# Kernel optimization log

Measured on AMD Instinct MI355X. Metric: run time of the kernel, lower is better.

## Reference

```python
import jax, jax.numpy as jnp
import numpy as np

B, S, D = 4, 2048, 1024
MULT = 4
INNER = MULT * D
E = 4          # n_expert
K = 1          # top-k
ALPHA = 0.5


def setup_inputs() -> dict:
    key = jax.random.key(0)
    ks = jax.random.split(key, 8)
    std = 0.02
    x = jax.random.normal(ks[0], (B, S, D), jnp.float32)
    W1 = jax.random.normal(ks[1], (D, INNER), jnp.float32) * std
    b1 = jnp.zeros((INNER,), jnp.float32)
    W2 = jax.random.normal(ks[2], (INNER, D), jnp.float32) * std
    b2 = jnp.zeros((D,), jnp.float32)
    Wg = jax.random.normal(ks[3], (D, E), jnp.float32) * std
    ew1 = jax.random.normal(ks[4], (E, D, INNER), jnp.float32) * std
    ew3 = jax.random.normal(ks[5], (E, D, INNER), jnp.float32) * std
    ew2 = jax.random.normal(ks[6], (E, INNER, D), jnp.float32) * std
    return {"x": x, "W1": W1, "b1": b1, "W2": W2, "b2": b2,
            "Wg": Wg, "ew1": ew1, "ew3": ew3, "ew2": ew2}


def reference(x, W1, b1, W2, b2, Wg, ew1, ew3, ew2):
    # Dense branch: Linear -> GELU (exact, torch default) -> Linear
    y_dense = jax.nn.gelu(x @ W1 + b1, approximate=False) @ W2 + b2

    # MoE branch: top-k softmax routing, SwiGLU experts
    logits = x @ Wg                                   # [B,S,E]
    probs = jax.nn.softmax(logits, axis=-1)
    topv, topi = jax.lax.top_k(probs, K)              # [B,S,K]
    gates = topv / jnp.sum(topv, axis=-1, keepdims=True)  # renormalize top-k
    onehot = jax.nn.one_hot(topi, E, dtype=x.dtype)   # [B,S,K,E]
    combine = jnp.sum(gates[..., None] * onehot, axis=-2)  # [B,S,E]

    y_moe = jnp.zeros_like(x)
    for e in range(E):  # small fixed expert count
        h = jax.nn.silu(x @ ew1[e]) * (x @ ew3[e])    # [B,S,INNER]
        y_moe = y_moe + combine[..., e:e + 1] * (h @ ew2[e])

    # Load-balancing aux loss: E * sum_e f_e * P_e
    frac = jnp.mean(jnp.sum(onehot, axis=-2), axis=(0, 1)) / K  # [E]
    pmean = jnp.mean(probs, axis=(0, 1))                        # [E]
    aux = E * jnp.sum(frac * pmean)

    y = ALPHA * y_dense + (1.0 - ALPHA) * y_moe
    return (y, aux)
```

## Files before the change

### kernel.cpp

```cpp
#include <hip/hip_runtime.h>
#include <hip/hip_bf16.h>


static constexpr int MT = 8192;
static constexpr int DD = 1024;
static constexpr int DI = 4096;

typedef float f32x4 __attribute__((ext_vector_type(4)));
typedef __bf16 bf16x8 __attribute__((ext_vector_type(8)));
typedef unsigned short u16;

__device__ __forceinline__ u16 f2bf(float f) {
    union { __hip_bfloat16 b; u16 u; } v;
    v.b = __float2bfloat16(f);
    return v.u;
}
__device__ __forceinline__ float bf2f(u16 u) {
    union { float f; unsigned i; } v;
    v.i = ((unsigned)u) << 16;
    return v.f;
}

__device__ __forceinline__ void gload_lds16(const void* g, void* l) {
    __builtin_amdgcn_global_load_lds(
        (const __attribute__((address_space(1))) void*)g,
        (__attribute__((address_space(3))) void*)l, 16, 0, 0);
}

__device__ __forceinline__ float gelu_f(float v) {
    return 0.5f * v * (1.0f + erff(v * 0.70710678118654752f));
}
__device__ __forceinline__ float silu_f(float v) {
    return v / (1.0f + expf(-v));
}

#define FENCE() asm volatile("" ::: "memory")
#define BARRIER() do { FENCE(); __builtin_amdgcn_s_barrier(); FENCE(); } while (0)
#define WAIT_LGKM0() asm volatile("s_waitcnt lgkmcnt(0)" ::: "memory")

__device__ __forceinline__ void transpose_tile(
    const float* __restrict__ s, u16* __restrict__ d, int K, int N,
    int pack, int packOff) {
    __shared__ u16 t[64][72];
    int n0 = blockIdx.x * 64, k0 = blockIdx.y * 64;
    int tid = threadIdx.x;
    int c = tid & 15;
    int r = tid >> 4;
#pragma unroll
    for (int p = 0; p < 4; ++p) {
        int k = r + p * 16;
        float4 v = *(const float4*)(s + (size_t)(k0 + k) * N + n0 + c * 4);
        t[c * 4 + 0][k] = f2bf(v.x);
        t[c * 4 + 1][k] = f2bf(v.y);
        t[c * 4 + 2][k] = f2bf(v.z);
        t[c * 4 + 3][k] = f2bf(v.w);
    }
    __syncthreads();
    int n = tid >> 2, kc = (tid & 3) * 16;
    const uint4* p0 = (const uint4*)&t[n][kc];
    uint4 a = p0[0], b = p0[1];
    int gn = n0 + n;
    int dr = pack ? ((gn >> 5) * 64 + (gn & 31) + packOff) : gn;
    uint4* o = (uint4*)(d + (size_t)dr * K + k0 + kc);
    o[0] = a; o[1] = b;
}

__global__ void __launch_bounds__(256) transpose_up(
    const float* __restrict__ W1, const float* __restrict__ ew1,
    const float* __restrict__ ew3, u16* __restrict__ W1t,
    u16* __restrict__ ew13t) {
    int z = blockIdx.z;
    if (z == 0) {
        transpose_tile(W1, W1t, DD, DI, 0, 0);
    } else if (z <= 4) {
        transpose_tile(ew1 + (size_t)(z - 1) * DD * DI,
                       ew13t + (size_t)(z - 1) * 2 * DD * DI, DD, DI, 1, 0);
    } else {
        transpose_tile(ew3 + (size_t)(z - 5) * DD * DI,
                       ew13t + (size_t)(z - 5) * 2 * DD * DI, DD, DI, 1, 32);
    }
}

__global__ void __launch_bounds__(256) transpose_dn(
    const float* __restrict__ W2, const float* __restrict__ ew2,
    u16* __restrict__ W2t, u16* __restrict__ ew2t) {
    int z = blockIdx.z;
    if (z == 0) {
        transpose_tile(W2, W2t, DI, DD, 0, 0);
    } else {
        transpose_tile(ew2 + (size_t)(z - 1) * DI * DD,
                       ew2t + (size_t)(z - 1) * DI * DD, DI, DD, 0, 0);
    }
}

__global__ void __launch_bounds__(256) gate_kernel(
    const float* __restrict__ x, const float* __restrict__ Wg,
    float* __restrict__ psum_blk, int* __restrict__ expertA) {
    int w = threadIdx.x >> 6, l = threadIdx.x & 63;
    int t = blockIdx.x * 4 + w;
    const float* xr = x + (size_t)t * DD;
    double a0 = 0, a1 = 0, a2 = 0, a3 = 0;
#pragma unroll
    for (int i = 0; i < 4; ++i) {
        int k = i * 256 + l * 4;
        float4 xv = *(const float4*)(xr + k);
        float4 w0 = *(const float4*)(Wg + (size_t)(k + 0) * 4);
        float4 w1 = *(const float4*)(Wg + (size_t)(k + 1) * 4);
        float4 w2 = *(const float4*)(Wg + (size_t)(k + 2) * 4);
        float4 w3 = *(const float4*)(Wg + (size_t)(k + 3) * 4);
        a0 += (double)xv.x * w0.x + (double)xv.y * w1.x + (double)xv.z * w2.x + (double)xv.w * w3.x;
        a1 += (double)xv.x * w0.y + (double)xv.y * w1.y + (double)xv.z * w2.y + (double)xv.w * w3.y;
        a2 += (double)xv.x * w0.z + (double)xv.y * w1.z + (double)xv.z * w2.z + (double)xv.w * w3.z;
        a3 += (double)xv.x * w0.w + (double)xv.y * w1.w + (double)xv.z * w2.w + (double)xv.w * w3.w;
    }
#pragma unroll
    for (int o = 32; o; o >>= 1) {
        a0 += __shfl_down(a0, o); a1 += __shfl_down(a1, o);
        a2 += __shfl_down(a2, o); a3 += __shfl_down(a3, o);
    }
    __shared__ float wps[4][4];
    if (l == 0) {
        double lg[4] = {a0, a1, a2, a3};
        int best = 0;
#pragma unroll
        for (int e = 1; e < 4; ++e) if (lg[e] > lg[best]) best = e;
        double m = lg[best], s = 0, p[4];
#pragma unroll
        for (int e = 0; e < 4; ++e) { p[e] = exp(lg[e] - m); s += p[e]; }
#pragma unroll
        for (int e = 0; e < 4; ++e) wps[w][e] = (float)(p[e] / s);
        expertA[t] = best;
    }
    __syncthreads();
    if (threadIdx.x < 4)
        psum_blk[blockIdx.x * 4 + threadIdx.x] =
            wps[0][threadIdx.x] + wps[1][threadIdx.x] + wps[2][threadIdx.x] + wps[3][threadIdx.x];
}

__global__ void __launch_bounds__(1024) build_lists(
    const int* __restrict__ expertA, const float* __restrict__ psum_blk,
    int* __restrict__ dstArr, int* __restrict__ rev,
    int* __restrict__ offsets, float* __restrict__ auxOut) {
    __shared__ int sc[4][1024];
    __shared__ float fs[1024];
    __shared__ float psum_s[4];
    __shared__ int tot_s[4], off_s[4];
    int tid = threadIdx.x;
    int le[8]; int c[4] = {0, 0, 0, 0};
#pragma unroll
    for (int i = 0; i < 8; ++i) { int e = expertA[tid * 8 + i]; le[i] = e; c[e]++; }
#pragma unroll
    for (int e = 0; e < 4; ++e) sc[e][tid] = c[e];
    __syncthreads();
    for (int o = 1; o < 1024; o <<= 1) {
        int v[4];
#pragma unroll
        for (int e = 0; e < 4; ++e) v[e] = (tid >= o) ? sc[e][tid - o] : 0;
        __syncthreads();
#pragma unroll
        for (int e = 0; e < 4; ++e) if (tid >= o) sc[e][tid] += v[e];
        __syncthreads();
    }
    if (tid == 0) {
        int o = 0;
#pragma unroll
        for (int e = 0; e < 4; ++e) {
            tot_s[e] = sc[e][1023]; off_s[e] = o; offsets[e] = o; o += tot_s[e];
        }
        offsets[4] = o;
    }
    __syncthreads();
    int base[4];
#pragma unroll
    for (int e = 0; e < 4; ++e) base[e] = off_s[e] + sc[e][tid] - c[e];
#pragma unroll
    for (int i = 0; i < 8; ++i) {
        int e = le[i]; int d = base[e]++; int t = tid * 8 + i;
        dstArr[t] = d; rev[d] = t;
    }
    float ps[4];
#pragma unroll
    for (int e = 0; e < 4; ++e)
        ps[e] = psum_blk[(2 * tid) * 4 + e] + psum_blk[(2 * tid + 1) * 4 + e];
    for (int e = 0; e < 4; ++e) {
        fs[tid] = ps[e]; __syncthreads();
        for (int o = 512; o; o >>= 1) { if (tid < o) fs[tid] += fs[tid + o]; __syncthreads(); }
        if (tid == 0) psum_s[e] = fs[0];
        __syncthreads();
    }
    if (tid == 0) {
        float a = 0;
#pragma unroll
        for (int e = 0; e < 4; ++e)
            a += ((float)tot_s[e] * (1.f / 8192.f)) * (psum_s[e] * (1.f / 8192.f));
        auxOut[0] = 4.f * a;
    }
}

__global__ void __launch_bounds__(256) gather_kernel(
    const float* __restrict__ x, const int* __restrict__ dstArr,
    u16* __restrict__ xg) {
    int w = threadIdx.x >> 6, l = threadIdx.x & 63;
    int t = blockIdx.x * 4 + w;
    int dst = dstArr[t];
    const float* xr = x + (size_t)t * DD;
#pragma unroll
    for (int i = 0; i < 4; ++i) {
        int k = i * 256 + l * 4;
        float4 v = *(const float4*)(xr + k);
        ushort4 u;
        u.x = f2bf(v.x); u.y = f2bf(v.y); u.z = f2bf(v.z); u.w = f2bf(v.w);
        *(ushort4*)(xg + (size_t)dst * DD + k) = u;
    }
}

template <int MODE, int NF>
__global__ void __launch_bounds__(512, 2) gemm8(
    const u16* __restrict__ A, const u16* __restrict__ Bw,
    const float* __restrict__ bias,
    u16* __restrict__ outB, float* __restrict__ outF,
    const int* __restrict__ offsets, const int* __restrict__ rev,
    int N, int K) {
    constexpr int BN   = NF * 64;
    constexpr int WCW  = NF * 16;
    constexpr int AELT = 2 * 256 * 32;
    constexpr int BUFE = AELT + 2 * BN * 32;
    constexpr int NIB  = NF / 2;
    __shared__ u16 lds[2 * BUFE];

    const int tid = threadIdx.x;
    const int w = tid >> 6, l = tid & 63;
    const int lr = l & 15, lg = l >> 4;
    const int wr = w >> 2, wc = w & 3;

    int rowBase, rowsValid = 256;
    const u16* Bp = Bw;
    if constexpr (MODE >= 2) {
        int e = blockIdx.z;
        int off = offsets[e], cnt = offsets[e + 1] - off;
        if ((int)blockIdx.y * 256 >= cnt) return;
        rowBase = off + blockIdx.y * 256;
        rowsValid = cnt - (int)blockIdx.y * 256;
        if (rowsValid > 256) rowsValid = 256;
        Bp = Bw + (size_t)e * ((size_t)2 * DD * DI);
    } else {
        rowBase = blockIdx.y * 256;
    }
    const int colBase = blockIdx.x * BN;
    const int NT = K >> 6;

    auto stageA = [&](int kt, int b, int ks) {
        const int kk = (kt << 6) + (ks << 5);
#pragma unroll
        for (int i = 0; i < 2; ++i) {
            int o = ((w << 1) + i) * 512 + (l << 3);
            int o2 = o ^ (((o >> 8) & 1) << 4);
            gload_lds16(A + (size_t)(rowBase + (o2 >> 5)) * K + kk + (o2 & 31),
                        &lds[b * BUFE + ks * 8192 + ((w << 1) + i) * 512]);
        }
    };
    auto stageB = [&](int kt, int b, int ks) {
        const int kk = (kt << 6) + (ks << 5);
#pragma unroll
        for (int i = 0; i < NIB; ++i) {
            int o = (w * NIB + i) * 512 + (l << 3);
            int o2 = o ^ (((o >> 8) & 1) << 4);
            gload_lds16(Bp + (size_t)(colBase + (o2 >> 5)) * K + kk + (o2 & 31),
                        &lds[b * BUFE + AELT + ks * (BN * 32) + (w * NIB + i) * 512]);
        }
    };

#define WAIT_VMB() do { \
    if constexpr (NF == 4) asm volatile("s_waitcnt vmcnt(4)" ::: "memory"); \
    else                   asm volatile("s_waitcnt vmcnt(3)" ::: "memory"); \
} while (0)

#define READBF(b_, ks_) do { \
    _Pragma("unroll") \
    for (int n = 0; n < NF; ++n) { \
        int e_ = (wc * WCW + n * 16 + lr) * 32 + lg * 8; \
        e_ ^= ((e_ >> 8) & 1) << 4; \
        bf[n] = *(const bf16x8*)&lds[(b_) * BUFE + AELT + (ks_) * (BN * 32) + e_]; \
    } \
} while (0)

#define READAF(b_, ks_, mq_) do { \
    _Pragma("unroll") \
    for (int m = 0; m < 4; ++m) { \
        int e_ = (wr * 128 + ((mq_) * 4 + m) * 16 + lr) * 32 + lg * 8; \
        e_ ^= ((e_ >> 8) & 1) << 4; \
        af[m] = *(const bf16x8*)&lds[(b_) * BUFE + (ks_) * 8192 + e_]; \
    } \
} while (0)

#define DOMFMA(mq_) do { \
    __builtin_amdgcn_s_setprio(1); \
    _Pragma("unroll") \
    for (int m = 0; m < 4; ++m) \
    _Pragma("unroll") \
    for (int n = 0; n < NF; ++n) \
        acc[(mq_) * 4 + m][n] = __builtin_amdgcn_mfma_f32_16x16x32_bf16( \
            bf[n], af[m], acc[(mq_) * 4 + m][n], 0, 0, 0); \
    __builtin_amdgcn_s_setprio(0); \
} while (0)

    f32x4 acc[8][NF];
#pragma unroll
    for (int m = 0; m < 8; ++m)
#pragma unroll
        for (int n = 0; n < NF; ++n) acc[m][n] = (f32x4){0.f, 0.f, 0.f, 0.f};
    bf16x8 af[4], bf[NF];

    stageA(0, 0, 0); stageB(0, 0, 0); stageA(0, 0, 1); stageB(0, 0, 1);
    stageA(1, 1, 0); stageB(1, 1, 0);
    WAIT_VMB();
    BARRIER();

    for (int t = 0; t < NT; ++t) {
        const int cb = t & 1, nb = cb ^ 1;
        const int tp1 = (t + 1 < NT) ? t + 1 : NT - 1;
        const int tp2 = (t + 2 < NT) ? t + 2 : NT - 1;
        READBF(cb, 0); READAF(cb, 0, 0); stageA(tp1, nb, 1);
        BARRIER(); WAIT_LGKM0(); DOMFMA(0); BARRIER();
        READAF(cb, 0, 1); stageB(tp1, nb, 1);
        BARRIER(); WAIT_LGKM0(); DOMFMA(1); BARRIER();
        READBF(cb, 1); READAF(cb, 1, 0); stageA(tp2, cb, 0);
        BARRIER(); WAIT_LGKM0(); DOMFMA(0); BARRIER();
        READAF(cb, 1, 1); stageB(tp2, cb, 0);
        BARRIER(); WAIT_LGKM0(); DOMFMA(1);
        WAIT_VMB();
        BARRIER();
    }

#pragma unroll
    for (int m = 0; m < 8; ++m) {
        int rloc = wr * 128 + m * 16 + lr;
        if (MODE >= 2 && rloc >= rowsValid) continue;
        size_t grow = (size_t)(rowBase + rloc);
        if constexpr (MODE == 2) {
#pragma unroll
            for (int n = 0; n < 2; ++n) {
                int col = (colBase >> 1) + wc * 32 + n * 16 + lg * 4;
                f32x4 v1 = acc[m][n], v3 = acc[m][n + 2];
                ushort4 u;
                u.x = f2bf(silu_f(v1[0]) * v3[0]);
                u.y = f2bf(silu_f(v1[1]) * v3[1]);
                u.z = f2bf(silu_f(v1[2]) * v3[2]);
                u.w = f2bf(silu_f(v1[3]) * v3[3]);
                *(ushort4*)(outB + grow * N + col) = u;
            }
        } else {
#pragma unroll
            for (int n = 0; n < NF; ++n) {
                int col = colBase + wc * WCW + n * 16 + lg * 4;
                f32x4 v = acc[m][n];
                f32x4 bb = *(const f32x4*)(bias + col);
                ushort4 u;
                u.x = f2bf(gelu_f(v[0] + bb[0]));
                u.y = f2bf(gelu_f(v[1] + bb[1]));
                u.z = f2bf(gelu_f(v[2] + bb[2]));
                u.w = f2bf(gelu_f(v[3] + bb[3]));
                *(ushort4*)(outB + grow * N + col) = u;
            }
        }
    }
#undef WAIT_VMB
#undef READBF
#undef READAF
#undef DOMFMA
}

__global__ void __launch_bounds__(256) gemm97sp(
    const u16* __restrict__ Ad, const u16* __restrict__ Ag,
    const u16* __restrict__ W2t, const u16* __restrict__ ew2t,
    u16* __restrict__ yA, float* __restrict__ y,
    const int* __restrict__ offsets, const int* __restrict__ rev) {
    __shared__ u16 ldsA[128 * 32];
    __shared__ u16 ldsB[128 * 32];
    int tid = threadIdx.x, w = tid >> 6, l = tid & 63;
    int wr = w >> 1, wc = w & 1;

    int wg = blockIdx.x;
    int c = wg & 7;
    int s = wg >> 3;
    int x = s & 7;
    int p = c + ((s >> 3) << 3);

    const u16* Ap;
    const u16* Bp;
    int rowBase, rowsValid = 128;
    bool dense = (p < 64);
    if (dense) {
        rowBase = p * 128;
        Ap = Ad; Bp = W2t;
    } else {
        int pm = p - 64;
        int e = pm >> 6, yl = pm & 63;
        int off = offsets[e], cnt = offsets[e + 1] - off;
        if (yl * 128 >= cnt) return;
        rowBase = off + yl * 128;
        rowsValid = cnt - yl * 128;
        if (rowsValid > 128) rowsValid = 128;
        Ap = Ag; Bp = ew2t + (size_t)e * DD * DI;
    }
    int colBase = x * 128;

    f32x4 acc[4][4];
#pragma unroll
    for (int m = 0; m < 4; ++m)
#pragma unroll
        for (int n = 0; n < 4; ++n) acc[m][n] = (f32x4){0.f, 0.f, 0.f, 0.f};

    int lr = l & 15, lg = l >> 4;
    int ar = l >> 2, ac = (l & 3) * 8;

#pragma unroll 1
    for (int kt = 0; kt < DI / 32; ++kt) {
        int k0 = kt << 5;
        const u16* ga = Ap + (size_t)(rowBase + w * 32 + ar) * DI + k0 + ac;
        gload_lds16(ga, &ldsA[(w * 32) * 32]);
        gload_lds16(ga + (size_t)16 * DI, &ldsA[(w * 32 + 16) * 32]);
        const u16* gb = Bp + (size_t)(colBase + w * 32 + ar) * DI + k0 + ac;
        gload_lds16(gb, &ldsB[(w * 32) * 32]);
        gload_lds16(gb + (size_t)16 * DI, &ldsB[(w * 32 + 16) * 32]);
        __syncthreads();
        bf16x8 af[4], bfr[4];
#pragma unroll
        for (int m = 0; m < 4; ++m)
            af[m] = *(const bf16x8*)&ldsA[(wr * 64 + m * 16 + lr) * 32 + lg * 8];
#pragma unroll
        for (int n = 0; n < 4; ++n)
            bfr[n] = *(const bf16x8*)&ldsB[(wc * 64 + n * 16 + lr) * 32 + lg * 8];
#pragma unroll
        for (int m = 0; m < 4; ++m)
#pragma unroll
            for (int n = 0; n < 4; ++n)
                acc[m][n] = __builtin_amdgcn_mfma_f32_16x16x32_bf16(
                    bfr[n], af[m], acc[m][n], 0, 0, 0);
        __syncthreads();
    }

#pragma unroll
    for (int m = 0; m < 4; ++m) {
        int rloc = wr * 64 + m * 16 + lr;
        if (rloc >= rowsValid) continue;
        int r = rowBase + rloc;
#pragma unroll
        for (int n = 0; n < 4; ++n) {
            int col = colBase + wc * 64 + n * 16 + lg * 4;
            f32x4 v = acc[m][n];
            if (dense) {
                ushort4 u;
                u.x = f2bf(v[0]); u.y = f2bf(v[1]);
                u.z = f2bf(v[2]); u.w = f2bf(v[3]);
                *(ushort4*)(yA + (size_t)r * DD + col) = u;
            } else {
                int tok = rev[r];
                f32x4 rr;
#pragma unroll
                for (int j = 0; j < 4; ++j) rr[j] = 0.5f * v[j];
                *(f32x4*)(y + (size_t)tok * DD + col) = rr;
            }
        }
    }
}

__global__ void __launch_bounds__(256) combine_kernel(
    const u16* __restrict__ yA, const float* __restrict__ b2,
    const int* __restrict__ rev, float* __restrict__ y) {
    int w = threadIdx.x >> 6, l = threadIdx.x & 63;
    int r = blockIdx.x * 4 + w;
    int tok = rev[r];
    const u16* ar = yA + (size_t)r * DD;
    float* yr = y + (size_t)tok * DD;
#pragma unroll
    for (int i = 0; i < 4; ++i) {
        int c = i * 256 + l * 4;
        ushort4 ua = *(const ushort4*)(ar + c);
        float4 bb = *(const float4*)(b2 + c);
        f32x4 o = *(f32x4*)(yr + c);
        o[0] += 0.5f * (bf2f(ua.x) + bb.x);
        o[1] += 0.5f * (bf2f(ua.y) + bb.y);
        o[2] += 0.5f * (bf2f(ua.z) + bb.z);
        o[3] += 0.5f * (bf2f(ua.w) + bb.w);
        *(f32x4*)(yr + c) = o;
    }
}

extern "C" void kernel_launch(void* const* d_in, const int* in_sizes, int n_in,
                              void* d_out, int out_size, void* d_ws, size_t ws_size,
                              hipStream_t stream) {
    const float* x   = (const float*)d_in[0];
    const float* W1  = (const float*)d_in[1];
    const float* b1  = (const float*)d_in[2];
    const float* W2  = (const float*)d_in[3];
    const float* b2  = (const float*)d_in[4];
    const float* Wg  = (const float*)d_in[5];
    const float* ew1 = (const float*)d_in[6];
    const float* ew3 = (const float*)d_in[7];
    const float* ew2 = (const float*)d_in[8];
    float* y = (float*)d_out;
    float* auxOut = y + (size_t)MT * DD;

    char* ws = (char*)d_ws;
    size_t off = 0;
    auto take = [&](size_t b) -> void* {
        void* p = ws + off;
        off += (b + 255) & ~(size_t)255;
        return p;
    };
    u16* W1t   = (u16*)take((size_t)DI * DD * 2);
    u16* W2t   = (u16*)take((size_t)DI * DD * 2);
    u16* ew2t  = (u16*)take((size_t)4 * DI * DD * 2);
    u16* xg    = (u16*)take((size_t)(MT + 256) * DD * 2);
    u16* hg    = (u16*)take((size_t)(MT + 256) * DI * 2);
    int* expertA  = (int*)take(MT * 4);
    int* dstArr   = (int*)take(MT * 4);
    int* revA     = (int*)take(MT * 4);
    float* psum_blk = (float*)take(2048 * 4 * 4);
    int* offsets  = (int*)take(64);
    size_t ew13Bytes = (size_t)4 * 2 * DI * DD * 2;
    size_t hdBytes   = (size_t)(MT + 256) * DI * 2;
    u16* ew13t = (u16*)take(ew13Bytes > hdBytes ? ew13Bytes : hdBytes);
    u16* hd    = ew13t;
    u16* yA = xg;

    if (ws_size < off) return;

    dim3 blk(256);
    transpose_up<<<dim3(DI / 64, DD / 64, 9), blk, 0, stream>>>(W1, ew1, ew3, W1t, ew13t);
    transpose_dn<<<dim3(DD / 64, DI / 64, 5), blk, 0, stream>>>(W2, ew2, W2t, ew2t);
    gate_kernel<<<2048, 256, 0, stream>>>(x, Wg, psum_blk, expertA);
    build_lists<<<1, 1024, 0, stream>>>(expertA, psum_blk, dstArr, revA, offsets, auxOut);
    gather_kernel<<<2048, 256, 0, stream>>>(x, dstArr, xg);
    gemm8<2, 4><<<dim3(2 * DI / 256, MT / 256, 4), dim3(512), 0, stream>>>(
        xg, ew13t, nullptr, hg, nullptr, offsets, nullptr, DI, DD);
    gemm8<0, 4><<<dim3(DI / 256, MT / 256), dim3(512), 0, stream>>>(
        xg, W1t, b1, hd, nullptr, nullptr, nullptr, DI, DD);
    gemm97sp<<<dim3(2560), blk, 0, stream>>>(
        hd, hg, W2t, ew2t, yA, y, offsets, revA);
    combine_kernel<<<2048, blk, 0, stream>>>(yA, b2, revA, y);
}
```

Before: 677.4 us.

## Rewrite down-projection GEMM with 256x128 tiles and double-buffered swizzled LDS pipeline

Replaces the simple 128x128 single-buffered down-projection GEMM with a 512-thread kernel using 256x128 tiles. It double-buffers the LDS, prefetches global-to-LDS loads two k-steps ahead, XOR-swizzles the LDS layout to cut bank conflicts, and raises MFMA priority. The aim is to hide global load latency behind compute and raise data reuse, following the structure of the existing up-projection kernel. The larger tiles waste more work on partially filled expert tiles, and the doubled LDS footprint plus the larger accumulator set may limit occupancy.

```diff
diff --git a/kernel.cpp b/kernel.cpp
--- a/kernel.cpp
+++ b/kernel.cpp
@@ -370,84 +370,129 @@
 #undef DOMFMA
 }
 
-__global__ void __launch_bounds__(256) gemm97sp(
-    const u16* __restrict__ Ad, const u16* __restrict__ Ag,
+__global__ void __launch_bounds__(512, 2) gemm8dn(
+    const u16* __restrict__ hd, const u16* __restrict__ hg,
     const u16* __restrict__ W2t, const u16* __restrict__ ew2t,
     u16* __restrict__ yA, float* __restrict__ y,
     const int* __restrict__ offsets, const int* __restrict__ rev) {
-    __shared__ u16 ldsA[128 * 32];
-    __shared__ u16 ldsB[128 * 32];
-    int tid = threadIdx.x, w = tid >> 6, l = tid & 63;
-    int wr = w >> 1, wc = w & 1;
+    constexpr int NF = 2;
+    constexpr int BN = 128;
+    constexpr int WCW = 32;
+    constexpr int AELT = 2 * 256 * 32;
+    constexpr int BUFE = AELT + 2 * BN * 32;
+    __shared__ u16 lds[2 * BUFE];
+
+    const int tid = threadIdx.x;
+    const int w = tid >> 6, l = tid & 63;
+    const int lr = l & 15, lg = l >> 4;
+    const int wr = w >> 2, wc = w & 3;
 
     int wg = blockIdx.x;
     int c = wg & 7;
     int s = wg >> 3;
     int x = s & 7;
-    int p = c + ((s >> 3) << 3);
-
+    int ps = c + ((s >> 3) << 3);
+    bool dense = (ps >= 128);
     const u16* Ap;
     const u16* Bp;
-    int rowBase, rowsValid = 128;
-    bool dense = (p < 64);
+    int rowBase, rowsValid = 256;
     if (dense) {
-        rowBase = p * 128;
-        Ap = Ad; Bp = W2t;
+        rowBase = (ps - 128) << 8;
+        Ap = hd; Bp = W2t;
     } else {
-        int pm = p - 64;
-        int e = pm >> 6, yl = pm & 63;
+        int e = ps >> 5, yl = ps & 31;
         int off = offsets[e], cnt = offsets[e + 1] - off;
-        if (yl * 128 >= cnt) return;
-        rowBase = off + yl * 128;
-        rowsValid = cnt - yl * 128;
-        if (rowsValid > 128) rowsValid = 128;
-        Ap = Ag; Bp = ew2t + (size_t)e * DD * DI;
-    }
-    int colBase = x * 128;
-
-    f32x4 acc[4][4];
-#pragma unroll
-    for (int m = 0; m < 4; ++m)
-#pragma unroll
-        for (int n = 0; n < 4; ++n) acc[m][n] = (f32x4){0.f, 0.f, 0.f, 0.f};
-
-    int lr = l & 15, lg = l >> 4;
-    int ar = l >> 2, ac = (l & 3) * 8;
-
-#pragma unroll 1
-    for (int kt = 0; kt < DI / 32; ++kt) {
-        int k0 = kt << 5;
-        const u16* ga = Ap + (size_t)(rowBase + w * 32 + ar) * DI + k0 + ac;
-        gload_lds16(ga, &ldsA[(w * 32) * 32]);
-        gload_lds16(ga + (size_t)16 * DI, &ldsA[(w * 32 + 16) * 32]);
-        const u16* gb = Bp + (size_t)(colBase + w * 32 + ar) * DI + k0 + ac;
-        gload_lds16(gb, &ldsB[(w * 32) * 32]);
-        gload_lds16(gb + (size_t)16 * DI, &ldsB[(w * 32 + 16) * 32]);
-        __syncthreads();
-        bf16x8 af[4], bfr[4];
-#pragma unroll
-        for (int m = 0; m < 4; ++m)
-            af[m] = *(const bf16x8*)&ldsA[(wr * 64 + m * 16 + lr) * 32 + lg * 8];
-#pragma unroll
-        for (int n = 0; n < 4; ++n)
-            bfr[n] = *(const bf16x8*)&ldsB[(wc * 64 + n * 16 + lr) * 32 + lg * 8];
-#pragma unroll
-        for (int m = 0; m < 4; ++m)
-#pragma unroll
-            for (int n = 0; n < 4; ++n)
-                acc[m][n] = __builtin_amdgcn_mfma_f32_16x16x32_bf16(
-                    bfr[n], af[m], acc[m][n], 0, 0, 0);
-        __syncthreads();
-    }
-
-#pragma unroll
-    for (int m = 0; m < 4; ++m) {
-        int rloc = wr * 64 + m * 16 + lr;
-        if (rloc >= rowsValid) continue;
+        if (yl * 256 >= cnt) return;
+        rowBase = off + yl * 256;
+        rowsValid = cnt - yl * 256;
+        if (rowsValid > 256) rowsValid = 256;
+        Ap = hg; Bp = ew2t + (size_t)e * DD * DI;
+    }
+    const int colBase = x * BN;
+    const int NT = DI >> 6;
+
+    auto stageA = [&](int kt, int b, int ks) {
+        const int kk = (kt << 6) + (ks << 5);
+#pragma unroll
+        for (int i = 0; i < 2; ++i) {
+            int o = ((w << 1) + i) * 512 + (l << 3);
+            int o2 = o ^ (((o >> 8) & 1) << 4);
+            gload_lds16(Ap + (size_t)(rowBase + (o2 >> 5)) * DI + kk + (o2 & 31),
+                        &lds[b * BUFE + ks * 8192 + ((w << 1) + i) * 512]);
+        }
+    };
+    auto stageB = [&](int kt, int b, int ks) {
+        const int kk = (kt << 6) + (ks << 5);
+        int o = w * 512 + (l << 3);
+        int o2 = o ^ (((o >> 8) & 1) << 4);
+        gload_lds16(Bp + (size_t)(colBase + (o2 >> 5)) * DI + kk + (o2 & 31),
+                    &lds[b * BUFE + AELT + ks * (BN * 32) + w * 512]);
+    };
+
+#define WAIT_VMB() asm volatile("s_waitcnt vmcnt(3)" ::: "memory")
+#define READBF(b_, ks_) do { \
+    _Pragma("unroll") \
+    for (int n = 0; n < NF; ++n) { \
+        int e_ = (wc * WCW + n * 16 + lr) * 32 + lg * 8; \
+        e_ ^= ((e_ >> 8) & 1) << 4; \
+        bf[n] = *(const bf16x8*)&lds[(b_) * BUFE + AELT + (ks_) * (BN * 32) + e_]; \
+    } \
+} while (0)
+#define READAF(b_, ks_, mq_) do { \
+    _Pragma("unroll") \
+    for (int m = 0; m < 4; ++m) { \
+        int e_ = (wr * 128 + ((mq_) * 4 + m) * 16 + lr) * 32 + lg * 8; \
+        e_ ^= ((e_ >> 8) & 1) << 4; \
+        af[m] = *(const bf16x8*)&lds[(b_) * BUFE + (ks_) * 8192 + e_]; \
+    } \
+} while (0)
+#define DOMFMA(mq_) do { \
+    __builtin_amdgcn_s_setprio(1); \
+    _Pragma("unroll") \
+    for (int m = 0; m < 4; ++m) \
+    _Pragma("unroll") \
+    for (int n = 0; n < NF; ++n) \
+        acc[(mq_) * 4 + m][n] = __builtin_amdgcn_mfma_f32_16x16x32_bf16( \
+            bf[n], af[m], acc[(mq_) * 4 + m][n], 0, 0, 0); \
+    __builtin_amdgcn_s_setprio(0); \
+} while (0)
+
+    f32x4 acc[8][NF];
+#pragma unroll
+    for (int m = 0; m < 8; ++m)
+#pragma unroll
+        for (int n = 0; n < NF; ++n) acc[m][n] = (f32x4){0.f, 0.f, 0.f, 0.f};
+    bf16x8 af[4], bf[NF];
+
+    stageA(0, 0, 0); stageB(0, 0, 0); stageA(0, 0, 1); stageB(0, 0, 1);
+    stageA(1, 1, 0); stageB(1, 1, 0);
+    WAIT_VMB();
+    BARRIER();
+
+    for (int t = 0; t < NT; ++t) {
+        const int cb = t & 1, nb = cb ^ 1;
+        const int tp1 = (t + 1 < NT) ? t + 1 : NT - 1;
+        const int tp2 = (t + 2 < NT) ? t + 2 : NT - 1;
+        READBF(cb, 0); READAF(cb, 0, 0); stageA(tp1, nb, 1);
+        BARRIER(); WAIT_LGKM0(); DOMFMA(0); BARRIER();
+        READAF(cb, 0, 1); stageB(tp1, nb, 1);
+        BARRIER(); WAIT_LGKM0(); DOMFMA(1); BARRIER();
+        READBF(cb, 1); READAF(cb, 1, 0); stageA(tp2, cb, 0);
+        BARRIER(); WAIT_LGKM0(); DOMFMA(0); BARRIER();
+        READAF(cb, 1, 1); stageB(tp2, cb, 0);
+        BARRIER(); WAIT_LGKM0(); DOMFMA(1);
+        WAIT_VMB();
+        BARRIER();
+    }
+
+#pragma unroll
+    for (int m = 0; m < 8; ++m) {
+        int rloc = wr * 128 + m * 16 + lr;
+        if (!dense && rloc >= rowsValid) continue;
         int r = rowBase + rloc;
 #pragma unroll
-        for (int n = 0; n < 4; ++n) {
-            int col = colBase + wc * 64 + n * 16 + lg * 4;
+        for (int n = 0; n < NF; ++n) {
+            int col = colBase + wc * WCW + n * 16 + lg * 4;
             f32x4 v = acc[m][n];
             if (dense) {
                 ushort4 u;
@@ -463,6 +508,10 @@
             }
         }
     }
+#undef WAIT_VMB
+#undef READBF
+#undef READAF
+#undef DOMFMA
 }
 
 __global__ void __launch_bounds__(256) combine_kernel(
@@ -537,7 +586,7 @@
         xg, ew13t, nullptr, hg, nullptr, offsets, nullptr, DI, DD);
     gemm8<0, 4><<<dim3(DI / 256, MT / 256), dim3(512), 0, stream>>>(
         xg, W1t, b1, hd, nullptr, nullptr, nullptr, DI, DD);
-    gemm97sp<<<dim3(2560), blk, 0, stream>>>(
+    gemm8dn<<<dim3(1280), dim3(512), 0, stream>>>(
         hd, hg, W2t, ew2t, yA, y, offsets, revA);
     combine_kernel<<<2048, blk, 0, stream>>>(yA, b2, revA, y);
 }
```

Result: faster. 574.2 us (-15.2%).
